# Performance work log

Measured on AMD Instinct MI355X. Metric: run time of the kernel, lower is better.

Reference implementation:

```python
import jax, jax.numpy as jnp
import numpy as np

N, E, DIN, DOUT = 40000, 640000, 128, 256
BN_EPS = 1e-5  # torch BatchNorm1d default eps


def setup_inputs() -> dict:
    key = jax.random.key(0)
    ks = jax.random.split(key, 16)
    x = jax.random.normal(ks[0], (N, DIN), jnp.float32)
    edge_index = jax.random.randint(ks[1], (2, E), 0, N, dtype=jnp.int32)
    s1 = 1.0 / np.sqrt(DIN)
    s2 = 1.0 / np.sqrt(DOUT)
    return {
        "x": x,
        "edge_index": edge_index,
        "eps": jnp.zeros((), jnp.float32),  # GINConv train_eps init = 0
        "W1": jax.random.normal(ks[2], (DIN, DOUT), jnp.float32) * s1,
        "b1": jnp.zeros((DOUT,), jnp.float32),
        "g1": jnp.ones((DOUT,), jnp.float32),
        "bt1": jnp.zeros((DOUT,), jnp.float32),
        "m1": jax.random.normal(ks[3], (DOUT,), jnp.float32) * 0.1,
        "v1": jax.random.uniform(ks[4], (DOUT,), jnp.float32, 0.5, 1.5),
        "W2": jax.random.normal(ks[5], (DOUT, DOUT), jnp.float32) * s2,
        "b2": jnp.zeros((DOUT,), jnp.float32),
        "g2": jnp.ones((DOUT,), jnp.float32),
        "bt2": jnp.zeros((DOUT,), jnp.float32),
        "m2": jax.random.normal(ks[6], (DOUT,), jnp.float32) * 0.1,
        "v2": jax.random.uniform(ks[7], (DOUT,), jnp.float32, 0.5, 1.5),
        "Wres": jax.random.normal(ks[8], (DIN, DOUT), jnp.float32) * s1,
    }


def _bn(h, g, b, m, v):
    # inference-mode BatchNorm1d with running stats
    return (h - m) * jax.lax.rsqrt(v + BN_EPS) * g + b


def reference(x, edge_index, eps, W1, b1, g1, bt1, m1, v1,
              W2, b2, g2, bt2, m2, v2, Wres):
    src, dst = edge_index[0], edge_index[1]
    # GIN sum aggregation: messages x[src] scatter-added at dst
    agg = jax.ops.segment_sum(x[src], dst, num_segments=N)  # [N, DIN]
    h = (1.0 + eps) * x + agg
    h = jax.nn.relu(_bn(h @ W1 + b1, g1, bt1, m1, v1))       # [N, DOUT]
    h = jax.nn.relu(_bn(h @ W2 + b2, g2, bt2, m2, v2))       # [N, DOUT]
    # dropout is identity in eval mode; residual projection since DIN != DOUT
    return jax.nn.relu(h + x @ Wres)
```

## Files before the change

### kernel.cpp

```cpp
#include <hip/hip_runtime.h>

#define NN 40000
#define NPAD 40064
#define EE 640000
#define KDIN 128
#define KDOUT 256

#define NBIN 157
#define BCAP 5120
#define CAPQ 1536

typedef __attribute__((ext_vector_type(8))) short bf16x8;
typedef __attribute__((ext_vector_type(4))) float f32x4;

static __device__ __forceinline__ unsigned short f2bf(float f) {
    union { float f; unsigned int u; } v; v.f = f;
    unsigned int r = (v.u + 0x7FFFu + ((v.u >> 16) & 1u)) >> 16;
    return (unsigned short)r;
}
static __device__ __forceinline__ float bf2f(unsigned short h) {
    union { unsigned int u; float f; } v; v.u = ((unsigned int)h) << 16;
    return v.f;
}

#define FRONT_GRID 3177
__global__ __launch_bounds__(256) void k_front(
    const float* __restrict__ x,
    const float* __restrict__ W1, const float* __restrict__ W2,
    const float* __restrict__ Wres, const int* __restrict__ ei,
    ushort* __restrict__ xb, ushort* __restrict__ wt_all,
    unsigned int* __restrict__ recs, int* __restrict__ lmat,
    ushort* __restrict__ hb) {
    __shared__ unsigned int SM[4096 + 480 + 256];
    int b = blockIdx.x, tid = threadIdx.x;
    if (b < NBIN) {
        unsigned int* lrec = SM;
        int* cnt    = (int*)(SM + 4096);
        int* lstart = cnt + 160;
        int* lcur   = lstart + 160;
        int* sw     = lcur + 160;
        int e0 = b * 4096;
        int ns = min(e0 + 4096, EE) - e0;

        if (tid < NBIN) cnt[tid] = 0;
        __syncthreads();
        for (int s = tid; s < ns; s += 256)
            atomicAdd(&cnt[ei[EE + e0 + s] >> 8], 1);
        __syncthreads();
        sw[tid] = (tid < NBIN) ? cnt[tid] : 0;
        __syncthreads();
        for (int off = 1; off < 256; off <<= 1) {
            int add = (tid >= off) ? sw[tid - off] : 0;
            __syncthreads();
            sw[tid] += add;
            __syncthreads();
        }
        if (tid < NBIN) {
            int st = sw[tid] - cnt[tid];
            lstart[tid] = st;
            lcur[tid] = st;
        }
        __syncthreads();
        for (int s = tid; s < ns; s += 256) {
            int e = e0 + s;
            int src = ei[e];
            int dst = ei[EE + e];
            int p = atomicAdd(&lcur[dst >> 8], 1);
            lrec[p] = ((unsigned int)(dst & 255) << 16) | (unsigned int)src;
        }
        __syncthreads();
        for (int s = tid; s < ns; s += 256)
            recs[b * 4096 + s] = lrec[s];
        if (tid < NBIN + 1)
            lmat[b * 158 + tid] = (tid < NBIN) ? lstart[tid] : ns;
    } else if (b < 2661) {
        int i = (b - NBIN) * 256 + tid;
        int row = i >> 4;
        uint4 o = {0, 0, 0, 0};
        if (row < NN) {
            const float4* xp = (const float4*)x + (size_t)i * 2;
            float4 a = xp[0], c = xp[1];
            o.x = (unsigned)f2bf(a.x) | ((unsigned)f2bf(a.y) << 16);
            o.y = (unsigned)f2bf(a.z) | ((unsigned)f2bf(a.w) << 16);
            o.z = (unsigned)f2bf(c.x) | ((unsigned)f2bf(c.y) << 16);
            o.w = (unsigned)f2bf(c.z) | ((unsigned)f2bf(c.w) << 16);
        }
        if (row < NPAD) *(uint4*)(xb + (size_t)i * 8) = o;
    } else if (b < 3173) {
        int j = (b - 2661) * 256 + tid;
        if (j < 32768) {
            int c = j >> 7, r = j & 127;
            wt_all[j] = f2bf(W1[r * KDOUT + c]);
        } else if (j < 98304) {
            int j2 = j - 32768;
            int c = j2 >> 8, r = j2 & 255;
            wt_all[j] = f2bf(W2[r * KDOUT + c]);
        } else {
            int j3 = j - 98304;
            int c = j3 >> 7, r = j3 & 127;
            wt_all[j] = f2bf(Wres[r * KDOUT + c]);
        }
    } else {
        int idx = (b - 3173) * 256 + tid;
        ((uint4*)(hb + (size_t)NN * KDIN))[idx] = (uint4){0, 0, 0, 0};
    }
}

__global__ __launch_bounds__(256) void k_aggB(const unsigned int* __restrict__ recs,
                                              const int* __restrict__ lmat,
                                              const ushort* __restrict__ xb,
                                              const float* __restrict__ eps,
                                              ushort* __restrict__ hb) {
    __shared__ unsigned int lrec[BCAP];
    __shared__ ushort lsrc[CAPQ];
    __shared__ int lcnt[64], lst[64], lcur[64];
    __shared__ int sw[256];
    int tid = threadIdx.x;
    int bi = blockIdx.x;
    int b = bi >> 4, nq = (bi >> 2) & 3, q = bi & 3;

    int len = 0, s0 = 0;
    if (tid < NBIN) {
        s0 = lmat[tid * 158 + b];
        len = lmat[tid * 158 + b + 1] - s0;
    }
    sw[tid] = len;
    __syncthreads();
    for (int off = 1; off < 256; off <<= 1) {
        int add = (tid >= off) ? sw[tid - off] : 0;
        __syncthreads();
        sw[tid] += add;
        __syncthreads();
    }
    int pofs = sw[tid] - len;
    int ctot = sw[255];
    for (int i = 0; i < len; ++i)
        lrec[pofs + i] = recs[tid * 4096 + s0 + i];
    if (tid < 64) lcnt[tid] = 0;
    __syncthreads();

    for (int s = tid; s < ctot; s += 256) {
        int d8 = lrec[s] >> 16;
        if ((d8 >> 6) == nq) atomicAdd(&lcnt[d8 & 63], 1);
    }
    __syncthreads();
    sw[tid] = (tid < 64) ? lcnt[tid] : 0;
    __syncthreads();
    for (int off = 1; off < 64; off <<= 1) {
        int add = (tid >= off) ? sw[tid - off] : 0;
        __syncthreads();
        sw[tid] += add;
        __syncthreads();
    }
    if (tid < 64) {
        int e = sw[tid] - lcnt[tid];
        lst[tid] = e;
        lcur[tid] = e;
    }
    __syncthreads();
    for (int s = tid; s < ctot; s += 256) {
        unsigned int r = lrec[s];
        int d8 = r >> 16;
        if ((d8 >> 6) == nq) {
            int p = atomicAdd(&lcur[d8 & 63], 1);
            lsrc[p] = (ushort)(r & 0xffff);
        }
    }
    __syncthreads();

    int g = tid >> 2, lane = tid & 3;
    int node = b * 256 + nq * 64 + g;
    if (node >= NN) return;
    float s1 = 1.0f + eps[0];
    int st = lst[g], en = st + lcnt[g];
    uint4 me = *((const uint4*)(xb + (size_t)node * KDIN) + q * 4 + lane);
    float a[8], a2[8];
    a[0] = bf2f((ushort)(me.x & 0xffff)) * s1; a[1] = bf2f((ushort)(me.x >> 16)) * s1;
    a[2] = bf2f((ushort)(me.y & 0xffff)) * s1; a[3] = bf2f((ushort)(me.y >> 16)) * s1;
    a[4] = bf2f((ushort)(me.z & 0xffff)) * s1; a[5] = bf2f((ushort)(me.z >> 16)) * s1;
    a[6] = bf2f((ushort)(me.w & 0xffff)) * s1; a[7] = bf2f((ushort)(me.w >> 16)) * s1;
#pragma unroll
    for (int i = 0; i < 8; ++i) a2[i] = 0.f;
    int e = st;
    for (; e + 1 < en; e += 2) {
        int sA = lsrc[e], sB = lsrc[e + 1];
        uint4 v0 = *((const uint4*)(xb + (size_t)sA * KDIN) + q * 4 + lane);
        uint4 v1 = *((const uint4*)(xb + (size_t)sB * KDIN) + q * 4 + lane);
        a[0] += bf2f((ushort)(v0.x & 0xffff)); a[1] += bf2f((ushort)(v0.x >> 16));
        a[2] += bf2f((ushort)(v0.y & 0xffff)); a[3] += bf2f((ushort)(v0.y >> 16));
        a[4] += bf2f((ushort)(v0.z & 0xffff)); a[5] += bf2f((ushort)(v0.z >> 16));
        a[6] += bf2f((ushort)(v0.w & 0xffff)); a[7] += bf2f((ushort)(v0.w >> 16));
        a2[0] += bf2f((ushort)(v1.x & 0xffff)); a2[1] += bf2f((ushort)(v1.x >> 16));
        a2[2] += bf2f((ushort)(v1.y & 0xffff)); a2[3] += bf2f((ushort)(v1.y >> 16));
        a2[4] += bf2f((ushort)(v1.z & 0xffff)); a2[5] += bf2f((ushort)(v1.z >> 16));
        a2[6] += bf2f((ushort)(v1.w & 0xffff)); a2[7] += bf2f((ushort)(v1.w >> 16));
    }
    if (e < en) {
        int sA = lsrc[e];
        uint4 v0 = *((const uint4*)(xb + (size_t)sA * KDIN) + q * 4 + lane);
        a[0] += bf2f((ushort)(v0.x & 0xffff)); a[1] += bf2f((ushort)(v0.x >> 16));
        a[2] += bf2f((ushort)(v0.y & 0xffff)); a[3] += bf2f((ushort)(v0.y >> 16));
        a[4] += bf2f((ushort)(v0.z & 0xffff)); a[5] += bf2f((ushort)(v0.z >> 16));
        a[6] += bf2f((ushort)(v0.w & 0xffff)); a[7] += bf2f((ushort)(v0.w >> 16));
    }
#pragma unroll
    for (int i = 0; i < 8; ++i) a[i] += a2[i];
    uint4 o;
    o.x = (unsigned)f2bf(a[0]) | ((unsigned)f2bf(a[1]) << 16);
    o.y = (unsigned)f2bf(a[2]) | ((unsigned)f2bf(a[3]) << 16);
    o.z = (unsigned)f2bf(a[4]) | ((unsigned)f2bf(a[5]) << 16);
    o.w = (unsigned)f2bf(a[6]) | ((unsigned)f2bf(a[7]) << 16);
    *((uint4*)(hb + (size_t)node * KDIN) + q * 4 + lane) = o;
}


#define STAGE_WT(Wt_, Kc_, K2_)                                                 \
    for (int id = tid; id < BNT * (K2_) / 16; id += 256) {                      \
        int c = id / ((K2_) / 16);                                              \
        int koff = (id % ((K2_) / 16)) * 16;                                    \
        uint4 v = *(const uint4*)((const char*)((Wt_) + (size_t)(ncol0 + c) * (Kc_)) + koff); \
        *(uint4*)((char*)s + c * (K2_) + (koff ^ ((c & 7) << 4))) = v;          \
    }

#define MM_LOOP(A_, Kc_, K2_, acc0_, acc1_)                                     \
    {                                                                           \
        const char* a0p = (const char*)((A_) + (size_t)r0 * (Kc_)) + lq * 16;   \
        const char* a1p = a0p + 16 * (Kc_) * 2;                                 \
        for (int k0 = 0; k0 < (Kc_); k0 += 32) {                                \
            bf16x8 a0 = *(const bf16x8*)(a0p + k0 * 2);                         \
            bf16x8 a1 = *(const bf16x8*)(a1p + k0 * 2);                         \
            int kb = (k0 + lq * 8) * 2;                                         \
            _Pragma("unroll")                                                   \
            for (int nt = 0; nt < 8; ++nt) {                                    \
                int c = nt * 16 + l15;                                          \
                bf16x8 b = *(const bf16x8*)((const char*)s + c * (K2_) + (kb ^ ((c & 7) << 4))); \
                acc0_[nt] = __builtin_amdgcn_mfma_f32_16x16x32_bf16(a0, b, acc0_[nt], 0, 0, 0); \
                acc1_[nt] = __builtin_amdgcn_mfma_f32_16x16x32_bf16(a1, b, acc1_[nt], 0, 0, 0); \
            }                                                                   \
        }                                                                       \
    }

#define BNT 128

__global__ __launch_bounds__(256) void k_mm1(
    const ushort* __restrict__ A, const ushort* __restrict__ Wt,
    const float* __restrict__ bb, const float* __restrict__ g,
    const float* __restrict__ bt, const float* __restrict__ m,
    const float* __restrict__ vv, ushort* __restrict__ C) {
    __shared__ ushort s[BNT * 128];
    int tid = threadIdx.x;
    int bm = blockIdx.x >> 1, bn = blockIdx.x & 1;
    int ncol0 = bn * BNT;
    STAGE_WT(Wt, 128, 256);
    __syncthreads();
    int wid = tid >> 6, lane = tid & 63;
    int l15 = lane & 15, lq = lane >> 4;
    int r0 = bm * 128 + wid * 32 + l15;
    f32x4 acc0[8] = {}, acc1[8] = {};
    MM_LOOP(A, 128, 256, acc0, acc1);
#pragma unroll
    for (int nt = 0; nt < 8; ++nt) {
        int col = ncol0 + nt * 16 + l15;
        float sc = g[col] * rsqrtf(vv[col] + 1e-5f);
        float bo = (bb[col] - m[col]) * sc + bt[col];
        int rb = bm * 128 + wid * 32 + lq * 4;
#pragma unroll
        for (int r = 0; r < 4; ++r) {
            C[(size_t)(rb + r) * KDOUT + col] = f2bf(fmaxf(acc0[nt][r] * sc + bo, 0.f));
            C[(size_t)(rb + 16 + r) * KDOUT + col] = f2bf(fmaxf(acc1[nt][r] * sc + bo, 0.f));
        }
    }
}

__global__ __launch_bounds__(256) void k_mm2(
    const ushort* __restrict__ H1, const ushort* __restrict__ W2t,
    const ushort* __restrict__ X, const ushort* __restrict__ Wrt,
    const float* __restrict__ bb, const float* __restrict__ g,
    const float* __restrict__ bt, const float* __restrict__ m,
    const float* __restrict__ vv, float* __restrict__ OUT) {
    __shared__ ushort s[BNT * 256];
    int tid = threadIdx.x;
    int bm = blockIdx.x >> 1, bn = blockIdx.x & 1;
    int ncol0 = bn * BNT;
    int wid = tid >> 6, lane = tid & 63;
    int l15 = lane & 15, lq = lane >> 4;
    int r0 = bm * 128 + wid * 32 + l15;

    STAGE_WT(W2t, 256, 512);
    __syncthreads();
    f32x4 acc0[8] = {}, acc1[8] = {};
    MM_LOOP(H1, 256, 512, acc0, acc1);

    __syncthreads();
    STAGE_WT(Wrt, 128, 256);
    __syncthreads();
    f32x4 acd0[8] = {}, acd1[8] = {};
    MM_LOOP(X, 128, 256, acd0, acd1);

#pragma unroll
    for (int nt = 0; nt < 8; ++nt) {
        int col = ncol0 + nt * 16 + l15;
        float sc = g[col] * rsqrtf(vv[col] + 1e-5f);
        float bo = (bb[col] - m[col]) * sc + bt[col];
        int rb = bm * 128 + wid * 32 + lq * 4;
#pragma unroll
        for (int r = 0; r < 4; ++r) {
            int row0 = rb + r, row1 = rb + 16 + r;
            float t0 = fmaxf(acc0[nt][r] * sc + bo, 0.f);
            float t1 = fmaxf(acc1[nt][r] * sc + bo, 0.f);
            if (row0 < NN) OUT[(size_t)row0 * KDOUT + col] = fmaxf(t0 + acd0[nt][r], 0.f);
            if (row1 < NN) OUT[(size_t)row1 * KDOUT + col] = fmaxf(t1 + acd1[nt][r], 0.f);
        }
    }
}

extern "C" void kernel_launch(void* const* d_in, const int* in_sizes, int n_in,
                              void* d_out, int out_size, void* d_ws, size_t ws_size,
                              hipStream_t stream) {
    const float* x    = (const float*)d_in[0];
    const int*   ei   = (const int*)d_in[1];
    const float* eps  = (const float*)d_in[2];
    const float* W1   = (const float*)d_in[3];
    const float* b1   = (const float*)d_in[4];
    const float* g1   = (const float*)d_in[5];
    const float* bt1  = (const float*)d_in[6];
    const float* m1   = (const float*)d_in[7];
    const float* v1   = (const float*)d_in[8];
    const float* W2   = (const float*)d_in[9];
    const float* b2   = (const float*)d_in[10];
    const float* g2   = (const float*)d_in[11];
    const float* bt2  = (const float*)d_in[12];
    const float* m2   = (const float*)d_in[13];
    const float* v2   = (const float*)d_in[14];
    const float* Wres = (const float*)d_in[15];
    float* out = (float*)d_out;

    char* w = (char*)d_ws;
    ushort* xb  = (ushort*)w;                 w += (size_t)NPAD * KDIN * 2;
    ushort* hb  = (ushort*)w;                 w += (size_t)NPAD * KDIN * 2;
    ushort* h1b = (ushort*)w;                 w += (size_t)NPAD * KDOUT * 2;
    ushort* w1t = (ushort*)w;                 w += 256 * 128 * 2;
    ushort* w2t = (ushort*)w;                 w += 256 * 256 * 2;
    ushort* wrt = (ushort*)w;                 w += 256 * 128 * 2;
    unsigned int* recs = (unsigned int*)w;    w += (size_t)NBIN * 4096 * 4;
    int* lmat   = (int*)w;                    w += (size_t)NBIN * 158 * 4;

    k_front<<<FRONT_GRID, 256, 0, stream>>>(x, W1, W2, Wres, ei, xb, w1t,
                                            recs, lmat, hb);
    k_aggB<<<NBIN * 16, 256, 0, stream>>>(recs, lmat, xb, eps, hb);

    const int grid = (NPAD / 128) * 2;
    k_mm1<<<grid, 256, 0, stream>>>(hb, w1t, b1, g1, bt1, m1, v1, h1b);
    k_mm2<<<grid, 256, 0, stream>>>(h1b, w2t, xb, wrt, b2, g2, bt2, m2, v2, out);
}
```

Measured before the change: 110.3 us.

## Halve aggregation blocks with 128-node halves and wave-cooperative record loading

The aggregation kernel now splits each 256-node bin into two halves of 128 nodes instead of four quarters of 64, and launches half as many blocks. Each thread handles two destination nodes. The per-bin record staging is also rewritten so each wave copies a source chunk with coalesced lanes, replacing the old scheme where one thread serially copied its whole chunk. This cuts the redundant re-reading and re-filtering of bin records across blocks, at the cost of fewer blocks and more shared memory per block.

```diff
diff --git a/kernel.cpp b/kernel.cpp
--- a/kernel.cpp
+++ b/kernel.cpp
@@ -8,7 +8,7 @@
 
 #define NBIN 157
 #define BCAP 5120
-#define CAPQ 1536
+#define HCAP 2816
 
 typedef __attribute__((ext_vector_type(8))) short bf16x8;
 typedef __attribute__((ext_vector_type(4))) float f32x4;
@@ -106,25 +106,22 @@
     }
 }
 
-__global__ __launch_bounds__(256) void k_aggB(const unsigned int* __restrict__ recs,
-                                              const int* __restrict__ lmat,
-                                              const ushort* __restrict__ xb,
-                                              const float* __restrict__ eps,
-                                              ushort* __restrict__ hb) {
+__global__ __launch_bounds__(256) void k_aggD(
+    const unsigned int* __restrict__ recs, const int* __restrict__ lmat,
+    const ushort* __restrict__ xb, const float* __restrict__ eps,
+    ushort* __restrict__ hb) {
     __shared__ unsigned int lrec[BCAP];
-    __shared__ ushort lsrc[CAPQ];
-    __shared__ int lcnt[64], lst[64], lcur[64];
+    __shared__ ushort lsrc[HCAP];
+    __shared__ int lcnt[128], lst[128], lcur[128];
     __shared__ int sw[256];
     int tid = threadIdx.x;
     int bi = blockIdx.x;
-    int b = bi >> 4, nq = (bi >> 2) & 3, q = bi & 3;
-
-    int len = 0, s0 = 0;
-    if (tid < NBIN) {
-        s0 = lmat[tid * 158 + b];
-        len = lmat[tid * 158 + b + 1] - s0;
-    }
-    sw[tid] = len;
+    int b = bi >> 3, nh = (bi >> 2) & 1, q = bi & 3;
+    int wid = tid >> 6, lane = tid & 63;
+
+    int len0 = 0;
+    if (tid < NBIN) len0 = lmat[tid * 158 + b + 1] - lmat[tid * 158 + b];
+    sw[tid] = len0;
     __syncthreads();
     for (int off = 1; off < 256; off <<= 1) {
         int add = (tid >= off) ? sw[tid - off] : 0;
@@ -132,27 +129,33 @@
         sw[tid] += add;
         __syncthreads();
     }
-    int pofs = sw[tid] - len;
     int ctot = sw[255];
-    for (int i = 0; i < len; ++i)
-        lrec[pofs + i] = recs[tid * 4096 + s0 + i];
-    if (tid < 64) lcnt[tid] = 0;
+
+    for (int c = wid; c < NBIN; c += 4) {
+        int s0 = lmat[c * 158 + b];
+        int len = lmat[c * 158 + b + 1] - s0;
+        int pofs = sw[c] - len;
+        const unsigned int* seg = recs + c * 4096 + s0;
+        for (int i = lane; i < len; i += 64)
+            lrec[pofs + i] = seg[i];
+    }
+    if (tid < 128) lcnt[tid] = 0;
     __syncthreads();
 
     for (int s = tid; s < ctot; s += 256) {
         int d8 = lrec[s] >> 16;
-        if ((d8 >> 6) == nq) atomicAdd(&lcnt[d8 & 63], 1);
-    }
-    __syncthreads();
-    sw[tid] = (tid < 64) ? lcnt[tid] : 0;
-    __syncthreads();
-    for (int off = 1; off < 64; off <<= 1) {
+        if ((d8 >> 7) == nh) atomicAdd(&lcnt[d8 & 127], 1);
+    }
+    __syncthreads();
+    sw[tid] = (tid < 128) ? lcnt[tid] : 0;
+    __syncthreads();
+    for (int off = 1; off < 128; off <<= 1) {
         int add = (tid >= off) ? sw[tid - off] : 0;
         __syncthreads();
         sw[tid] += add;
         __syncthreads();
     }
-    if (tid < 64) {
+    if (tid < 128) {
         int e = sw[tid] - lcnt[tid];
         lst[tid] = e;
         lcur[tid] = e;
@@ -161,56 +164,59 @@
     for (int s = tid; s < ctot; s += 256) {
         unsigned int r = lrec[s];
         int d8 = r >> 16;
-        if ((d8 >> 6) == nq) {
-            int p = atomicAdd(&lcur[d8 & 63], 1);
+        if ((d8 >> 7) == nh) {
+            int p = atomicAdd(&lcur[d8 & 127], 1);
             lsrc[p] = (ushort)(r & 0xffff);
         }
     }
     __syncthreads();
 
-    int g = tid >> 2, lane = tid & 3;
-    int node = b * 256 + nq * 64 + g;
-    if (node >= NN) return;
+    int g = tid >> 2, lane4 = tid & 3;
     float s1 = 1.0f + eps[0];
-    int st = lst[g], en = st + lcnt[g];
-    uint4 me = *((const uint4*)(xb + (size_t)node * KDIN) + q * 4 + lane);
-    float a[8], a2[8];
-    a[0] = bf2f((ushort)(me.x & 0xffff)) * s1; a[1] = bf2f((ushort)(me.x >> 16)) * s1;
-    a[2] = bf2f((ushort)(me.y & 0xffff)) * s1; a[3] = bf2f((ushort)(me.y >> 16)) * s1;
-    a[4] = bf2f((ushort)(me.z & 0xffff)) * s1; a[5] = bf2f((ushort)(me.z >> 16)) * s1;
-    a[6] = bf2f((ushort)(me.w & 0xffff)) * s1; a[7] = bf2f((ushort)(me.w >> 16)) * s1;
-#pragma unroll
-    for (int i = 0; i < 8; ++i) a2[i] = 0.f;
-    int e = st;
-    for (; e + 1 < en; e += 2) {
-        int sA = lsrc[e], sB = lsrc[e + 1];
-        uint4 v0 = *((const uint4*)(xb + (size_t)sA * KDIN) + q * 4 + lane);
-        uint4 v1 = *((const uint4*)(xb + (size_t)sB * KDIN) + q * 4 + lane);
-        a[0] += bf2f((ushort)(v0.x & 0xffff)); a[1] += bf2f((ushort)(v0.x >> 16));
-        a[2] += bf2f((ushort)(v0.y & 0xffff)); a[3] += bf2f((ushort)(v0.y >> 16));
-        a[4] += bf2f((ushort)(v0.z & 0xffff)); a[5] += bf2f((ushort)(v0.z >> 16));
-        a[6] += bf2f((ushort)(v0.w & 0xffff)); a[7] += bf2f((ushort)(v0.w >> 16));
-        a2[0] += bf2f((ushort)(v1.x & 0xffff)); a2[1] += bf2f((ushort)(v1.x >> 16));
-        a2[2] += bf2f((ushort)(v1.y & 0xffff)); a2[3] += bf2f((ushort)(v1.y >> 16));
-        a2[4] += bf2f((ushort)(v1.z & 0xffff)); a2[5] += bf2f((ushort)(v1.z >> 16));
-        a2[6] += bf2f((ushort)(v1.w & 0xffff)); a2[7] += bf2f((ushort)(v1.w >> 16));
-    }
-    if (e < en) {
-        int sA = lsrc[e];
-        uint4 v0 = *((const uint4*)(xb + (size_t)sA * KDIN) + q * 4 + lane);
-        a[0] += bf2f((ushort)(v0.x & 0xffff)); a[1] += bf2f((ushort)(v0.x >> 16));
-        a[2] += bf2f((ushort)(v0.y & 0xffff)); a[3] += bf2f((ushort)(v0.y >> 16));
-        a[4] += bf2f((ushort)(v0.z & 0xffff)); a[5] += bf2f((ushort)(v0.z >> 16));
-        a[6] += bf2f((ushort)(v0.w & 0xffff)); a[7] += bf2f((ushort)(v0.w >> 16));
-    }
-#pragma unroll
-    for (int i = 0; i < 8; ++i) a[i] += a2[i];
-    uint4 o;
-    o.x = (unsigned)f2bf(a[0]) | ((unsigned)f2bf(a[1]) << 16);
-    o.y = (unsigned)f2bf(a[2]) | ((unsigned)f2bf(a[3]) << 16);
-    o.z = (unsigned)f2bf(a[4]) | ((unsigned)f2bf(a[5]) << 16);
-    o.w = (unsigned)f2bf(a[6]) | ((unsigned)f2bf(a[7]) << 16);
-    *((uint4*)(hb + (size_t)node * KDIN) + q * 4 + lane) = o;
+    for (int it = 0; it < 2; ++it) {
+        int d = g + it * 64;
+        int node = b * 256 + nh * 128 + d;
+        if (node >= NN) continue;
+        int st = lst[d], en = st + lcnt[d];
+        uint4 me = *((const uint4*)(xb + (size_t)node * KDIN) + q * 4 + lane4);
+        float a[8], a2[8];
+        a[0] = bf2f((ushort)(me.x & 0xffff)) * s1; a[1] = bf2f((ushort)(me.x >> 16)) * s1;
+        a[2] = bf2f((ushort)(me.y & 0xffff)) * s1; a[3] = bf2f((ushort)(me.y >> 16)) * s1;
+        a[4] = bf2f((ushort)(me.z & 0xffff)) * s1; a[5] = bf2f((ushort)(me.z >> 16)) * s1;
+        a[6] = bf2f((ushort)(me.w & 0xffff)) * s1; a[7] = bf2f((ushort)(me.w >> 16)) * s1;
+#pragma unroll
+        for (int i = 0; i < 8; ++i) a2[i] = 0.f;
+        int e = st;
+        for (; e + 1 < en; e += 2) {
+            int sA = lsrc[e], sB = lsrc[e + 1];
+            uint4 v0 = *((const uint4*)(xb + (size_t)sA * KDIN) + q * 4 + lane4);
+            uint4 v1 = *((const uint4*)(xb + (size_t)sB * KDIN) + q * 4 + lane4);
+            a[0] += bf2f((ushort)(v0.x & 0xffff)); a[1] += bf2f((ushort)(v0.x >> 16));
+            a[2] += bf2f((ushort)(v0.y & 0xffff)); a[3] += bf2f((ushort)(v0.y >> 16));
+            a[4] += bf2f((ushort)(v0.z & 0xffff)); a[5] += bf2f((ushort)(v0.z >> 16));
+            a[6] += bf2f((ushort)(v0.w & 0xffff)); a[7] += bf2f((ushort)(v0.w >> 16));
+            a2[0] += bf2f((ushort)(v1.x & 0xffff)); a2[1] += bf2f((ushort)(v1.x >> 16));
+            a2[2] += bf2f((ushort)(v1.y & 0xffff)); a2[3] += bf2f((ushort)(v1.y >> 16));
+            a2[4] += bf2f((ushort)(v1.z & 0xffff)); a2[5] += bf2f((ushort)(v1.z >> 16));
+            a2[6] += bf2f((ushort)(v1.w & 0xffff)); a2[7] += bf2f((ushort)(v1.w >> 16));
+        }
+        if (e < en) {
+            int sA = lsrc[e];
+            uint4 v0 = *((const uint4*)(xb + (size_t)sA * KDIN) + q * 4 + lane4);
+            a[0] += bf2f((ushort)(v0.x & 0xffff)); a[1] += bf2f((ushort)(v0.x >> 16));
+            a[2] += bf2f((ushort)(v0.y & 0xffff)); a[3] += bf2f((ushort)(v0.y >> 16));
+            a[4] += bf2f((ushort)(v0.z & 0xffff)); a[5] += bf2f((ushort)(v0.z >> 16));
+            a[6] += bf2f((ushort)(v0.w & 0xffff)); a[7] += bf2f((ushort)(v0.w >> 16));
+        }
+#pragma unroll
+        for (int i = 0; i < 8; ++i) a[i] += a2[i];
+        uint4 o;
+        o.x = (unsigned)f2bf(a[0]) | ((unsigned)f2bf(a[1]) << 16);
+        o.y = (unsigned)f2bf(a[2]) | ((unsigned)f2bf(a[3]) << 16);
+        o.z = (unsigned)f2bf(a[4]) | ((unsigned)f2bf(a[5]) << 16);
+        o.w = (unsigned)f2bf(a[6]) | ((unsigned)f2bf(a[7]) << 16);
+        *((uint4*)(hb + (size_t)node * KDIN) + q * 4 + lane4) = o;
+    }
 }
 
 
@@ -347,7 +353,7 @@
 
     k_front<<<FRONT_GRID, 256, 0, stream>>>(x, W1, W2, Wres, ei, xb, w1t,
                                             recs, lmat, hb);
-    k_aggB<<<NBIN * 16, 256, 0, stream>>>(recs, lmat, xb, eps, hb);
+    k_aggD<<<NBIN * 8, 256, 0, stream>>>(recs, lmat, xb, eps, hb);
 
     const int grid = (NPAD / 128) * 2;
     k_mm1<<<grid, 256, 0, stream>>>(hb, w1t, b1, g1, bt1, m1, v1, h1b);
```

After: 114.8 us. +4.1%, slower.
